# Kernel tuning notes

Hardware: AMD Instinct MI355X
Metric: run time of the kernel (lower is better)

## Reference

```python
import jax, jax.numpy as jnp
from jax import lax
import numpy as np

PERCENTAGES = [0.004, 0.006, 0.008, 0.01, 0.012]
RADIUS = 1.0  # shape == 'square'
B, N = 4, 8192


def setup_inputs() -> dict:
    key = jax.random.key(0)
    adv_pcs = jax.random.uniform(key, (B, N, 3), dtype=jnp.float32)
    return {"adv_pcs": adv_pcs}


def _gather_points(pcs, idx):
    # pcs [B,N,3], idx [B,S] -> [B,S,3]
    idx3 = jnp.broadcast_to(idx[:, :, None], idx.shape + (3,))
    return jnp.take_along_axis(pcs, idx3, axis=1)


def farthest_point_sample(pcs, n_samples):
    # iterative FPS starting at index 0; returns indices [B, n_samples]
    Bb, Nn, _ = pcs.shape

    def step(carry, _):
        min_d2, last = carry  # [B,N], [B]
        p = _gather_points(pcs, last[:, None])  # [B,1,3]
        d2 = jnp.sum((pcs - p) ** 2, axis=-1)  # [B,N]
        min_d2 = jnp.minimum(min_d2, d2)
        nxt = jnp.argmax(min_d2, axis=-1).astype(jnp.int32)
        return (min_d2, nxt), last

    init = (jnp.full((Bb, Nn), 1e10, pcs.dtype), jnp.zeros((Bb,), jnp.int32))
    _, idx = lax.scan(step, init, None, length=n_samples)
    return jnp.transpose(idx)  # [B, n_samples]


def ball_query(seeds, pcs, r, K):
    # seeds [B,S,3], pcs [B,N,3] -> pts [B,S,K,3], idx [B,S,K] (-1 padded)
    d2 = jnp.sum((seeds[:, :, None, :] - pcs[:, None, :, :]) ** 2, axis=-1)  # [B,S,N]
    valid = d2 < r * r
    # stable sort: in-radius points first, preserving index order
    order = jnp.argsort(jnp.where(valid, 0, 1).astype(jnp.int32), axis=-1, stable=True)
    idx = order[..., :K]  # [B,S,K]
    cnt = jnp.sum(valid, axis=-1)  # [B,S]
    keep = jnp.arange(K)[None, None, :] < cnt[:, :, None]
    idx = jnp.where(keep, idx, -1)
    pts = jax.vmap(lambda p, i: p[i])(pcs, jnp.clip(idx, 0))  # [B,S,K,3]
    return pts, idx


def knn_second_sqdist(groups, lengths):
    # groups [G,K,3]; first `lengths[g]` rows of each group are valid candidates.
    # Returns squared distance to the 2nd nearest neighbor (incl. self at 0) [G,K].
    G, K, _ = groups.shape
    d2 = jnp.sum((groups[:, :, None, :] - groups[:, None, :, :]) ** 2, axis=-1)  # [G,K,K]
    col_ok = jnp.arange(K)[None, None, :] < lengths[:, None, None]
    d2 = jnp.where(col_ok, d2, jnp.inf)
    top2 = -lax.top_k(-d2, 2)[0]  # two smallest along candidates
    nn2 = top2[:, :, 1]  # second smallest (first is self, dist 0)
    return jnp.where(jnp.isfinite(nn2), nn2, 0.0)  # pad like pytorch3d (0 for missing)


def reference(adv_pcs):
    Bb, Nn, _ = adv_pcs.shape
    dt = adv_pcs.dtype
    seed_num = int(Nn * 0.05)
    fps_idx = farthest_point_sample(adv_pcs, seed_num)
    seeds = _gather_points(adv_pcs, fps_idx)  # [B,seed,3]
    loss = jnp.zeros((Bb,), dt)
    for p in PERCENTAGES:
        exp_num = Nn * p
        r = float(np.sqrt(p) * RADIUS)
        expect_dis = jnp.sqrt(jnp.asarray(np.pi * RADIUS ** 2 / exp_num * p, dt))
        K = int(2 * exp_num)
        pts, idx = ball_query(seeds, adv_pcs, r, K)
        pts = pts.reshape(Bb * seed_num, K, 3)
        idx = idx.reshape(Bb * seed_num, K)
        mask = idx != -1  # [G,K]
        gnum = jnp.sum(mask, axis=-1)  # [G], >= 1 (seed itself in-radius)
        nn2 = knn_second_sqdist(pts, gnum)  # [G,K] squared dists
        safe = jnp.where(nn2 > 0, nn2, 1.0)
        nn_dis = jnp.where(nn2 > 0, jnp.sqrt(safe), 0.0)
        clutter = jnp.square(nn_dis - expect_dis) / (expect_dis + 1e-12)
        # faithful to torch: sum over ALL elements, then elementwise divide by counts
        clutter_vec = jnp.sum(clutter * mask) / gnum.astype(dt)  # [G]
        imbalance = jnp.square(gnum.astype(dt) - exp_num) / exp_num  # [G]
        ul = (clutter_vec * imbalance).reshape(Bb, seed_num).mean(axis=-1)  # [B]
        loss = loss + ul
    return loss / len(PERCENTAGES)
```

## Files before the change

### kernel.cpp

```cpp
#include <hip/hip_runtime.h>
#include <math.h>

#define N_PTS 8192
#define B_SZ 4
#define SEED_NUM 409
#define THREADS 256
#define LTOT 653
#define N_GROUPS (B_SZ * SEED_NUM)
#define PUB 16

typedef float f2 __attribute__((ext_vector_type(2)));
typedef float f4 __attribute__((ext_vector_type(4)));

__device__ __forceinline__ float sqdist(float ax, float ay, float az,
                                        float bx, float by, float bz) {
  float dx = __fsub_rn(ax, bx);
  float dy = __fsub_rn(ay, by);
  float dz = __fsub_rn(az, bz);
  return __fadd_rn(__fadd_rn(__fmul_rn(dx, dx), __fmul_rn(dy, dy)),
                   __fmul_rn(dz, dz));
}

#define FOR16(M) \
  M(0) M(1) M(2) M(3) M(4) M(5) M(6) M(7) \
  M(8) M(9) M(10) M(11) M(12) M(13) M(14) M(15)

template <int CTRL>
__device__ __forceinline__ unsigned long long dpp_u64_bc1(
    unsigned long long k) {
  const unsigned lo2 = (unsigned)__builtin_amdgcn_update_dpp(
      0, (int)(unsigned)k, CTRL, 0xf, 0xf, true);
  const unsigned hi2 = (unsigned)__builtin_amdgcn_update_dpp(
      0, (int)(unsigned)(k >> 32), CTRL, 0xf, 0xf, true);
  return ((unsigned long long)hi2 << 32) | lo2;
}
template <int CTRL, int ROW_MASK>
__device__ __forceinline__ unsigned long long dpp_u64_keep(
    unsigned long long k) {
  const unsigned lo2 = (unsigned)__builtin_amdgcn_update_dpp(
      (int)(unsigned)k, (int)(unsigned)k, CTRL, ROW_MASK, 0xf, false);
  const unsigned hi2 = (unsigned)__builtin_amdgcn_update_dpp(
      (int)(unsigned)(k >> 32), (int)(unsigned)(k >> 32), CTRL, ROW_MASK, 0xf,
      false);
  return ((unsigned long long)hi2 << 32) | lo2;
}

struct FpsSmem {
  f4 spts4[N_PTS];
  float seedbuf[SEED_NUM * 3];
  unsigned long long red[2][4];
};
struct GrpSmem {
  f4 tmp[LTOT];
  f4 lpt[LTOT];
  int tcnt[5], tbase[5], bcnt[5], ccum[5];
  int ntmp, capped;
  int wtot[4];
  double wsum[5][4];
  float ssd[3];
  int islast;
};
union SmemU {
  FpsSmem f;
  GrpSmem g;
};

__global__ __launch_bounds__(THREADS, 1) void fused_kernel(
    const float* __restrict__ pcs, float* __restrict__ seeds,
    double* __restrict__ sums ,
    unsigned int* __restrict__ ctr ,
    float* __restrict__ out) {
#pragma clang fp contract(off)
  const int tid = threadIdx.x;
  __shared__ SmemU sm;
  __shared__ int roleS;
  __shared__ double fin[25];

  if (tid == 0) roleS = (int)atomicAdd(&ctr[0], 1u);
  __syncthreads();
  const int role = roleS;

  if (role < B_SZ) {
    const int b = role;
    const int lane = tid & 63, wid = tid >> 6;
    const float* base = pcs + (size_t)b * N_PTS * 3;
    f4* spts4 = sm.f.spts4;
    float* seedbuf = sm.f.seedbuf;
    auto& red = sm.f.red;

#define FPS_DECL(j) f2 px##j, py##j, pz##j, md##j;
    FOR16(FPS_DECL)
#undef FPS_DECL

#define FPS_INIT(j)                                   \
  {                                                   \
    const int i0 = tid + (2 * (j)) * THREADS;         \
    const int i1 = i0 + THREADS;                      \
    px##j = (f2){base[i0 * 3 + 0], base[i1 * 3 + 0]}; \
    py##j = (f2){base[i0 * 3 + 1], base[i1 * 3 + 1]}; \
    pz##j = (f2){base[i0 * 3 + 2], base[i1 * 3 + 2]}; \
    md##j = (f2){1e10f, 1e10f};   \
    spts4[i0] = (f4){px##j.x, py##j.x, pz##j.x, 0.f}; \
    spts4[i1] = (f4){px##j.y, py##j.y, pz##j.y, 0.f}; \
  }
    FOR16(FPS_INIT)
#undef FPS_INIT

#define FPS_PIN(j) asm volatile("" : "+v"(px##j), "+v"(py##j), "+v"(pz##j));
    FOR16(FPS_PIN)
#undef FPS_PIN

    float cx = base[0], cy = base[1], cz = base[2];

    for (int s = 0; s < SEED_NUM; ++s) {
      if (tid == 0) {
        seedbuf[s * 3 + 0] = cx;
        seedbuf[s * 3 + 1] = cy;
        seedbuf[s * 3 + 2] = cz;
        if ((s & (PUB - 1)) == (PUB - 1)) {
          const int s0 = s - (PUB - 1);
          float* sg = seeds + ((size_t)b * SEED_NUM + s0) * 3;
          for (int i = 0; i < PUB * 3; ++i)
            atomicExch(&sg[i], seedbuf[s0 * 3 + i]);
          __hip_atomic_store(&ctr[2 + b], (unsigned)(s + 1),
                             __ATOMIC_RELEASE, __HIP_MEMORY_SCOPE_AGENT);
        }
      }
      const f2 ccx = (f2){cx, cx}, ccy = (f2){cy, cy}, ccz = (f2){cz, cz};
      float bv = -1.0f;
      int bi = 0;
#define FPS_UPD(j)                                                  \
  {                                                                 \
    const f2 dx = px##j - ccx;                                      \
    const f2 dy = py##j - ccy;                                      \
    const f2 dz = pz##j - ccz;                                      \
    const f2 t0 = dx * dx;                                          \
    const f2 t1 = dy * dy;                                          \
    const f2 t2 = dz * dz;                                          \
    const f2 d2 = (t0 + t1) + t2;                                   \
    const f2 m = __builtin_elementwise_min(md##j, d2);              \
    md##j = m;                                                      \
    if (m.x > bv) { bv = m.x; bi = tid + (2 * (j)) * THREADS; }     \
    if (m.y > bv) { bv = m.y; bi = tid + (2 * (j) + 1) * THREADS; } \
  }
      FOR16(FPS_UPD)
#undef FPS_UPD
      unsigned long long key =
          ((unsigned long long)__float_as_uint(bv) << 32) |
          (unsigned long long)(unsigned)(N_PTS - 1 - bi);
      unsigned long long o;
      o = dpp_u64_bc1<0x111>(key);        key = (o > key) ? o : key;
      o = dpp_u64_bc1<0x112>(key);        key = (o > key) ? o : key;
      o = dpp_u64_bc1<0x114>(key);        key = (o > key) ? o : key;
      o = dpp_u64_bc1<0x118>(key);        key = (o > key) ? o : key;
      o = dpp_u64_keep<0x142, 0xa>(key);  key = (o > key) ? o : key;
      o = dpp_u64_keep<0x143, 0xc>(key);  key = (o > key) ? o : key;
      if (lane == 63) red[s & 1][wid] = key;
      __syncthreads();
      unsigned long long kmax = red[s & 1][0];
#pragma unroll
      for (int w = 1; w < 4; ++w) {
        const unsigned long long t = red[s & 1][w];
        kmax = (t > kmax) ? t : kmax;
      }
      const int ci = N_PTS - 1 - (int)(unsigned)(kmax & 0xffffffffull);
      const f4 c = spts4[ci];
      cx = c.x;
      cy = c.y;
      cz = c.z;
    }

    if (tid == 0) {
      const int s0 = SEED_NUM & ~(PUB - 1);
      float* sg = seeds + ((size_t)b * SEED_NUM + s0) * 3;
      for (int i = 0; i < (SEED_NUM - s0) * 3; ++i)
        atomicExch(&sg[i], seedbuf[s0 * 3 + i]);
      __hip_atomic_store(&ctr[2 + b], (unsigned)SEED_NUM, __ATOMIC_RELEASE,
                         __HIP_MEMORY_SCOPE_AGENT);
    }
    return;
  }

  const int tk = role - B_SZ;
  if (tk >= N_GROUPS) return;
  const int s = tk >> 2;
  const int b = tk & 3;
  const int lane = tid & 63, wid = tid >> 6;

  const int Kc[5] = {65, 98, 131, 163, 196};
  const int off[5] = {0, 65, 163, 294, 457};
  const double Pd[5] = {0.004, 0.006, 0.008, 0.01, 0.012};
  float r2c[5], expnf[5], expdc[5];
#pragma unroll
  for (int p = 0; p < 5; ++p) {
    const double pd = Pd[p];
    const double rd = sqrt(pd);
    r2c[p] = (float)(rd * rd);
    const double expn_d = 8192.0 * pd;
    expnf[p] = (float)expn_d;
    expdc[p] = sqrtf((float)(M_PI / expn_d * pd));
  }

  const float* base = pcs + (size_t)b * N_PTS * 3;
  f4* tmp = sm.g.tmp;
  f4* lpt = sm.g.lpt;
  int* tcnt = sm.g.tcnt;
  int* tbase = sm.g.tbase;
  int* bcnt = sm.g.bcnt;
  int* ccum = sm.g.ccum;
  int* wtot = sm.g.wtot;
  double (*wsum)[4] = sm.g.wsum;
  double* totS = sums;
  double* accA = sums + 5;

  if (tid < 5) { tcnt[tid] = 0; bcnt[tid] = 0; }
  if (tid == 6) sm.g.ntmp = 0;
  if (tid == 0) {
    while (__hip_atomic_load(&ctr[2 + b], __ATOMIC_ACQUIRE,
                             __HIP_MEMORY_SCOPE_AGENT) <= (unsigned)s)
      __builtin_amdgcn_s_sleep(16);
    const size_t so = ((size_t)b * SEED_NUM + s) * 3;
    sm.g.ssd[0] = atomicAdd(&seeds[so + 0], 0.0f);
    sm.g.ssd[1] = atomicAdd(&seeds[so + 1], 0.0f);
    sm.g.ssd[2] = atomicAdd(&seeds[so + 2], 0.0f);
  }
  __syncthreads();
  const float sx = sm.g.ssd[0], sy = sm.g.ssd[1], sz = sm.g.ssd[2];

  const float r2max = r2c[4];
  const f4* base4 = (const f4*)base;
#define PROC(X, Y, Z)                                              \
  {                                                                \
    const float d2 = sqdist((X), (Y), (Z), sx, sy, sz);            \
    if (d2 < r2max) {                                              \
      const int tier = (d2 < r2c[0]) ? 0                           \
                       : (d2 < r2c[1]) ? 1                         \
                       : (d2 < r2c[2]) ? 2                         \
                       : (d2 < r2c[3]) ? 3 : 4;                    \
      atomicAdd(&tcnt[tier], 1);                                   \
      const int pos = atomicAdd(&sm.g.ntmp, 1);                    \
      if (pos < LTOT) tmp[pos] = (f4){(X), (Y), (Z), (float)tier}; \
    }                                                              \
  }
  for (int it = 0; it < 8; ++it) {
    const int q = it * 256 + tid;
    const f4 v0 = base4[q * 3 + 0];
    const f4 v1 = base4[q * 3 + 1];
    const f4 v2 = base4[q * 3 + 2];
    PROC(v0.x, v0.y, v0.z)
    PROC(v0.w, v1.x, v1.y)
    PROC(v1.z, v1.w, v2.x)
    PROC(v2.y, v2.z, v2.w)
  }
#undef PROC
  __syncthreads();

  if (tid == 0) {
    int acc = 0, cap = 0;
#pragma unroll
    for (int t = 0; t < 5; ++t) {
      tbase[t] = acc;
      acc += tcnt[t];
      ccum[t] = acc;
    }
#pragma unroll
    for (int p = 0; p < 5; ++p) cap |= (ccum[p] > Kc[p]) ? 1 : 0;
    sm.g.capped = cap;
  }
  __syncthreads();

  const int nt = min(sm.g.ntmp, LTOT);
  for (int t = tid; t < nt; t += 256) {
    const f4 e = tmp[t];
    const int tier = (int)e.w;
    const int pos = tbase[tier] + atomicAdd(&bcnt[tier], 1);
    if (pos < LTOT) lpt[pos] = (f4){e.x, e.y, e.z, 0.f};
  }
  __syncthreads();

  if (!sm.g.capped) {
    const int c0 = ccum[0], c1 = ccum[1], c2 = ccum[2], c3 = ccum[3],
              c4 = ccum[4];
    double lS0 = 0.0, lS1 = 0.0, lS2 = 0.0, lS3 = 0.0, lS4 = 0.0;
    for (int r0 = 0; r0 < c4; r0 += 64) {
      const int row = r0 + (tid >> 2);
      const int sub = tid & 3;
      const bool rok = row < c4;
      const f4 pi = lpt[rok ? row : 0];
      float m1 = INFINITY, m2 = INFINITY;
      int j = sub;
#define SEGMENT(CP, EDP, LSP)                                        \
  {                                                                  \
    for (; j < (CP); j += 4) {                                       \
      const f4 pj = lpt[j];                                          \
      const float d2 = sqdist(pi.x, pi.y, pi.z, pj.x, pj.y, pj.z);   \
      if (d2 < m1) { m2 = m1; m1 = d2; }                             \
      else if (d2 < m2) { m2 = d2; }                                 \
    }                                                                \
    float s1 = m1, s2 = m2;                                          \
    {                                                                \
      const float o1 = __shfl_xor(s1, 1), o2 = __shfl_xor(s2, 1);    \
      const float lo = fminf(s1, o1), hi = fmaxf(s1, o1);            \
      s2 = fminf(fminf(s2, o2), hi); s1 = lo;                        \
    }                                                                \
    {                                                                \
      const float o1 = __shfl_xor(s1, 2), o2 = __shfl_xor(s2, 2);    \
      const float lo = fminf(s1, o1), hi = fmaxf(s1, o1);            \
      s2 = fminf(fminf(s2, o2), hi); s1 = lo;                        \
    }                                                                \
    if (rok && sub == 0 && row < (CP)) {                             \
      const float nn2 = (s2 > 1e37f) ? 0.0f : s2;      \
      const float nnd = (nn2 > 0.0f) ? sqrtf(nn2) : 0.0f;            \
      const float diff = __fsub_rn(nnd, (EDP));                      \
      const float clut = __fdiv_rn(__fmul_rn(diff, diff),            \
                                   __fadd_rn((EDP), 1e-12f));        \
      LSP += (double)clut;                                           \
    }                                                                \
  }
      SEGMENT(c0, expdc[0], lS0)
      SEGMENT(c1, expdc[1], lS1)
      SEGMENT(c2, expdc[2], lS2)
      SEGMENT(c3, expdc[3], lS3)
      SEGMENT(c4, expdc[4], lS4)
#undef SEGMENT
    }
#define RED(LSP, P)                                          \
  {                                                          \
    double v = (LSP);                                        \
    for (int o = 32; o > 0; o >>= 1) v += __shfl_down(v, o); \
    if (lane == 0) wsum[(P)][wid] = v;                       \
  }
    RED(lS0, 0) RED(lS1, 1) RED(lS2, 2) RED(lS3, 3) RED(lS4, 4)
#undef RED
  } else {
#pragma unroll
    for (int p = 0; p < 5; ++p) {
      int run = 0;
      for (int base_i = 0; base_i < N_PTS; base_i += 256) {
        const int i = base_i + tid;
        const float x = base[i * 3 + 0];
        const float y = base[i * 3 + 1];
        const float z = base[i * 3 + 2];
        const float d2 = sqdist(x, y, z, sx, sy, sz);
        const bool valid = d2 < r2c[p];
        const unsigned long long m = __ballot(valid);
        if (lane == 0) wtot[wid] = __popcll(m);
        __syncthreads();
        int pos = run + __popcll(m & ((1ull << lane) - 1ull));
        for (int w = 0; w < wid; ++w) pos += wtot[w];
        if (valid && pos < Kc[p]) {
          lpt[off[p] + pos] = (f4){x, y, z, 0.f};
        }
        run += wtot[0] + wtot[1] + wtot[2] + wtot[3];
        __syncthreads();
      }
    }
#pragma unroll
    for (int p = 0; p < 5; ++p) {
      const int gn = min(ccum[p], Kc[p]);
      const float ed = expdc[p];
      const int lb = off[p];
      double localS = 0.0;
      for (int r0 = 0; r0 < gn; r0 += 64) {
        const int row = r0 + (tid >> 2);
        const int sub = tid & 3;
        float m1 = INFINITY, m2 = INFINITY;
        if (row < gn) {
          const f4 pi = lpt[lb + row];
          for (int j = sub; j < gn; j += 4) {
            const f4 pj = lpt[lb + j];
            const float d2 = sqdist(pi.x, pi.y, pi.z, pj.x, pj.y, pj.z);
            if (d2 < m1) { m2 = m1; m1 = d2; }
            else if (d2 < m2) { m2 = d2; }
          }
        }
#pragma unroll
        for (int d = 1; d <= 2; d <<= 1) {
          const float om1 = __shfl_xor(m1, d);
          const float om2 = __shfl_xor(m2, d);
          const float lo = fminf(m1, om1);
          const float hi = fmaxf(m1, om1);
          m2 = fminf(fminf(m2, om2), hi);
          m1 = lo;
        }
        if (row < gn && sub == 0) {
          const float nn2 = (m2 > 1e37f) ? 0.0f : m2;
          const float nnd = (nn2 > 0.0f) ? sqrtf(nn2) : 0.0f;
          const float diff = __fsub_rn(nnd, ed);
          const float clut = __fdiv_rn(__fmul_rn(diff, diff),
                                       __fadd_rn(ed, 1e-12f));
          localS += (double)clut;
        }
      }
#pragma unroll
      for (int o = 32; o > 0; o >>= 1) localS += __shfl_down(localS, o);
      if (lane == 0) wsum[p][wid] = localS;
      __syncthreads();
    }
  }
  __syncthreads();

  if (tid < 5) {
    const double S = wsum[tid][0] + wsum[tid][1] + wsum[tid][2] + wsum[tid][3];
    atomicAdd(&totS[tid], S);
  } else if (tid < 10) {
    const int p = tid - 5;
    const int gn = min(ccum[p], Kc[p]);
    const float gf = (float)gn;
    const float dd = __fsub_rn(gf, expnf[p]);
    const float imb = __fdiv_rn(__fmul_rn(dd, dd), expnf[p]);
    atomicAdd(&accA[p * 4 + b], (double)imb / (double)gf);
  }

  __syncthreads();
  if (tid == 0) {
    __threadfence();
    const unsigned int old = atomicAdd(&ctr[1], 1u);
    sm.g.islast = (old == (unsigned int)(N_GROUPS - 1)) ? 1 : 0;
  }
  __syncthreads();
  if (sm.g.islast) {
    if (tid < 25) {
      double* src = (tid < 5) ? &totS[tid] : &accA[tid - 5];
      fin[tid] = atomicAdd(src, 0.0);
    }
    __syncthreads();
    if (tid < B_SZ) {
      double acc = 0.0;
#pragma unroll
      for (int p = 0; p < 5; ++p)
        acc += fin[p] * (fin[5 + p * 4 + tid] / (double)SEED_NUM);
      out[tid] = (float)(acc / 5.0);
    }
  }
}

extern "C" void kernel_launch(void* const* d_in, const int* in_sizes, int n_in,
                              void* d_out, int out_size, void* d_ws,
                              size_t ws_size, hipStream_t stream) {
  (void)in_sizes; (void)n_in; (void)out_size; (void)ws_size;
  const float* pcs = (const float*)d_in[0];
  float* out = (float*)d_out;

  float* seeds = (float*)d_ws;
  double* sums = (double*)((char*)d_ws + 19632);
  unsigned int* ctr = (unsigned int*)((char*)d_ws + 19632 + 200);

  hipMemsetAsync((char*)d_ws + 19632, 0, 200 + 24, stream);
  fused_kernel<<<B_SZ + N_GROUPS, THREADS, 0, stream>>>(pcs, seeds, sums, ctr,
                                                        out);
}
```

Measured before the change: 479.0 us.

## Parallelize seed publishing and pad progress counters to separate cache lines

Seed publication from the FPS blocks moves off a serial loop on thread 0 and is spread across 48 threads, and it is deferred by one chunk so the stores overlap the reduction barrier. The role, done and per-batch progress counters are each padded onto their own 128-byte region to reduce false sharing between the FPS producers and the polling consumer blocks. The consumer poll sleep is also lengthened. The aim is to shorten the FPS critical path and cut contention on the counters, at the cost of consumers seeing seeds up to one chunk later.

```diff
diff --git a/kernel.cpp b/kernel.cpp
--- a/kernel.cpp
+++ b/kernel.cpp
@@ -8,6 +8,10 @@
 #define LTOT 653
 #define N_GROUPS (B_SZ * SEED_NUM)
 #define PUB 16
+
+#define CTR_ROLE 0
+#define CTR_DONE 32
+#define CTR_PROG(b) (64 + 32 * (b))
 
 typedef float f2 __attribute__((ext_vector_type(2)));
 typedef float f4 __attribute__((ext_vector_type(4)));
@@ -76,7 +80,7 @@
   __shared__ int roleS;
   __shared__ double fin[25];
 
-  if (tid == 0) roleS = (int)atomicAdd(&ctr[0], 1u);
+  if (tid == 0) roleS = (int)atomicAdd(&ctr[CTR_ROLE], 1u);
   __syncthreads();
   const int role = roleS;
 
@@ -87,6 +91,7 @@
     f4* spts4 = sm.f.spts4;
     float* seedbuf = sm.f.seedbuf;
     auto& red = sm.f.red;
+    float* sgb = seeds + (size_t)b * SEED_NUM * 3;
 
 #define FPS_DECL(j) f2 px##j, py##j, pz##j, md##j;
     FOR16(FPS_DECL)
@@ -117,14 +122,11 @@
         seedbuf[s * 3 + 0] = cx;
         seedbuf[s * 3 + 1] = cy;
         seedbuf[s * 3 + 2] = cz;
-        if ((s & (PUB - 1)) == (PUB - 1)) {
-          const int s0 = s - (PUB - 1);
-          float* sg = seeds + ((size_t)b * SEED_NUM + s0) * 3;
-          for (int i = 0; i < PUB * 3; ++i)
-            atomicExch(&sg[i], seedbuf[s0 * 3 + i]);
-          __hip_atomic_store(&ctr[2 + b], (unsigned)(s + 1),
-                             __ATOMIC_RELEASE, __HIP_MEMORY_SCOPE_AGENT);
-        }
+      }
+      const bool pubit = (s != 0) && ((s & (PUB - 1)) == 0);
+      if (pubit && tid < PUB * 3) {
+        const float v = seedbuf[(s - PUB) * 3 + tid];
+        atomicExch(&sgb[(s - PUB) * 3 + tid], v);
       }
       const f2 ccx = (f2){cx, cx}, ccy = (f2){cy, cy}, ccz = (f2){cz, cz};
       float bv = -1.0f;
@@ -157,6 +159,10 @@
       o = dpp_u64_keep<0x143, 0xc>(key);  key = (o > key) ? o : key;
       if (lane == 63) red[s & 1][wid] = key;
       __syncthreads();
+      if (pubit && tid == 0) {
+        __hip_atomic_store(&ctr[CTR_PROG(b)], (unsigned)s, __ATOMIC_RELEASE,
+                           __HIP_MEMORY_SCOPE_AGENT);
+      }
       unsigned long long kmax = red[s & 1][0];
 #pragma unroll
       for (int w = 1; w < 4; ++w) {
@@ -170,13 +176,17 @@
       cz = c.z;
     }
 
-    if (tid == 0) {
+    {
       const int s0 = SEED_NUM & ~(PUB - 1);
-      float* sg = seeds + ((size_t)b * SEED_NUM + s0) * 3;
-      for (int i = 0; i < (SEED_NUM - s0) * 3; ++i)
-        atomicExch(&sg[i], seedbuf[s0 * 3 + i]);
-      __hip_atomic_store(&ctr[2 + b], (unsigned)SEED_NUM, __ATOMIC_RELEASE,
-                         __HIP_MEMORY_SCOPE_AGENT);
+      const int nfl = (SEED_NUM - s0) * 3;
+      if (tid < nfl) {
+        const float v = seedbuf[s0 * 3 + tid];
+        atomicExch(&sgb[s0 * 3 + tid], v);
+      }
+      __syncthreads();
+      if (tid == 0)
+        __hip_atomic_store(&ctr[CTR_PROG(b)], (unsigned)SEED_NUM,
+                           __ATOMIC_RELEASE, __HIP_MEMORY_SCOPE_AGENT);
     }
     return;
   }
@@ -216,9 +226,9 @@
   if (tid < 5) { tcnt[tid] = 0; bcnt[tid] = 0; }
   if (tid == 6) sm.g.ntmp = 0;
   if (tid == 0) {
-    while (__hip_atomic_load(&ctr[2 + b], __ATOMIC_ACQUIRE,
+    while (__hip_atomic_load(&ctr[CTR_PROG(b)], __ATOMIC_ACQUIRE,
                              __HIP_MEMORY_SCOPE_AGENT) <= (unsigned)s)
-      __builtin_amdgcn_s_sleep(16);
+      __builtin_amdgcn_s_sleep(32);
     const size_t so = ((size_t)b * SEED_NUM + s) * 3;
     sm.g.ssd[0] = atomicAdd(&seeds[so + 0], 0.0f);
     sm.g.ssd[1] = atomicAdd(&seeds[so + 1], 0.0f);
@@ -415,7 +425,7 @@
   __syncthreads();
   if (tid == 0) {
     __threadfence();
-    const unsigned int old = atomicAdd(&ctr[1], 1u);
+    const unsigned int old = atomicAdd(&ctr[CTR_DONE], 1u);
     sm.g.islast = (old == (unsigned int)(N_GROUPS - 1)) ? 1 : 0;
   }
   __syncthreads();
@@ -444,9 +454,9 @@
 
   float* seeds = (float*)d_ws;
   double* sums = (double*)((char*)d_ws + 19632);
-  unsigned int* ctr = (unsigned int*)((char*)d_ws + 19632 + 200);
-
-  hipMemsetAsync((char*)d_ws + 19632, 0, 200 + 24, stream);
+  unsigned int* ctr = (unsigned int*)((char*)d_ws + 19840);
+
+  hipMemsetAsync((char*)d_ws + 19632, 0, 976, stream);
   fused_kernel<<<B_SZ + N_GROUPS, THREADS, 0, stream>>>(pcs, seeds, sums, ctr,
                                                         out);
 }
```

After: 444.1 us. 7.3% less time.
